# Optimization experiments

Hardware: AMD Instinct MI355X
Metric: run time of the kernel (lower is better)

Reference implementation:

```python
import jax, jax.numpy as jnp
import numpy as np

D_MODEL = 1024
D_FF = 4096
NUM_EXPERTS = 8
TOP_K = 2


def setup_inputs() -> dict:
    key = jax.random.key(0)
    ks = jax.random.split(key, 7)
    s = 1.0 / np.sqrt(D_MODEL)
    sf = 1.0 / np.sqrt(D_FF)
    x = jax.random.normal(ks[0], (4, 2048, D_MODEL), dtype=jnp.float32)
    gate_w = jax.random.uniform(ks[1], (D_MODEL, NUM_EXPERTS), minval=-s, maxval=s, dtype=jnp.float32)
    gate_b = jnp.zeros((NUM_EXPERTS,), dtype=jnp.float32)
    w1 = jax.random.uniform(ks[2], (NUM_EXPERTS, D_MODEL, D_FF), minval=-s, maxval=s, dtype=jnp.float32)
    b1 = jax.random.uniform(ks[3], (NUM_EXPERTS, D_FF), minval=-s, maxval=s, dtype=jnp.float32)
    w2 = jax.random.uniform(ks[4], (NUM_EXPERTS, D_FF, D_MODEL), minval=-sf, maxval=sf, dtype=jnp.float32)
    b2 = jax.random.uniform(ks[5], (NUM_EXPERTS, D_MODEL), minval=-sf, maxval=sf, dtype=jnp.float32)
    return {"x": x, "gate_w": gate_w, "gate_b": gate_b, "w1": w1, "b1": b1, "w2": w2, "b2": b2}


def reference(x, gate_w, gate_b, w1, b1, w2, b2):
    # Router: softmax over experts, then top-k with renormalization.
    router_logits = jnp.einsum('bsd,de->bse', x, gate_w) + gate_b  # [B,S,E]
    router_probs = jax.nn.softmax(router_logits, axis=-1)
    topk_probs, topk_idx = jax.lax.top_k(router_probs, TOP_K)      # [B,S,K]
    topk_probs = topk_probs / jnp.sum(topk_probs, axis=-1, keepdims=True)

    # Dense combine weights: comb[b,s,e] = sum_k topk_probs[b,s,k] * (topk_idx[b,s,k]==e)
    one_hot = jax.nn.one_hot(topk_idx, NUM_EXPERTS, dtype=x.dtype)  # [B,S,K,E]
    comb = jnp.einsum('bsk,bske->bse', topk_probs, one_hot)         # [B,S,E]

    # Loop over the small fixed expert set; weight unselected experts by 0.
    out = jnp.zeros_like(x)
    for e in range(NUM_EXPERTS):
        h = jax.nn.relu(jnp.einsum('bsd,df->bsf', x, w1[e]) + b1[e])
        y = jnp.einsum('bsf,fd->bsd', h, w2[e]) + b2[e]
        out = out + comb[..., e:e + 1] * y

    # Routing statistics (same math as the torch module).
    expert_usage = jnp.mean(one_hot, axis=(0, 1, 2))  # fraction of (token,k) slots per expert
    avg_probs = jnp.mean(router_probs, axis=(0, 1))
    load_balance_loss = jnp.var(avg_probs, ddof=1)    # torch.var is unbiased by default
    return out, expert_usage, load_balance_loss
```

## Files before the change

### kernel.cpp

```cpp
#include <hip/hip_runtime.h>
#include <hip/hip_bf16.h>
#include <stdint.h>

#define D_MODEL 1024
#define D_FF    4096
#define NE      8
#define NTOK    8192
#define OUT_MAIN (NTOK * D_MODEL)

typedef float f32x4 __attribute__((ext_vector_type(4)));
typedef short s16x8 __attribute__((ext_vector_type(8)));

struct __align__(8) bh4 { __hip_bfloat16 x, y, z, w; };

static const size_t OFF_E12   = 4096;
static const size_t OFF_PFR   = 36864;
static const size_t OFF_ATOK  = 102400;
static const size_t OFF_AP    = 167936;
static const size_t OFF_XB    = 262144;
static const size_t OFF_W1T   = OFF_XB  + (size_t)NTOK * D_MODEL * 2;
static const size_t OFF_W2T   = OFF_W1T + (size_t)NE * D_MODEL * D_FF * 2;
static const size_t OFF_H     = OFF_W2T + (size_t)NE * D_MODEL * D_FF * 2;

__device__ inline void gll16(const void* g, void* lds) {
  __builtin_amdgcn_global_load_lds((__attribute__((address_space(1))) void*)g,
                                   (__attribute__((address_space(3))) void*)lds,
                                   16, 0, 0);
}

__global__ __launch_bounds__(256) void cvt_transpose_kernel(
    const float* __restrict__ src, __hip_bfloat16* __restrict__ dst, int K, int N)
{
  __shared__ __hip_bfloat16 tile[64][68];
  const int e = blockIdx.z;
  const float* s = src + (size_t)e * K * N;
  __hip_bfloat16* d = dst + (size_t)e * K * N;
  const int n0 = blockIdx.x * 64, k0 = blockIdx.y * 64;
  const int t = threadIdx.x;
#pragma unroll
  for (int i = 0; i < 4; ++i) {
    int q = i * 256 + t;
    int r = q >> 4, c4 = (q & 15) * 4;
    float4 v = *(const float4*)(s + (size_t)(k0 + r) * N + n0 + c4);
    tile[r][c4 + 0] = __float2bfloat16(v.x);
    tile[r][c4 + 1] = __float2bfloat16(v.y);
    tile[r][c4 + 2] = __float2bfloat16(v.z);
    tile[r][c4 + 3] = __float2bfloat16(v.w);
  }
  __syncthreads();
  const int n = t >> 2, c = (t & 3) * 16;
  __align__(16) __hip_bfloat16 tmp[16];
#pragma unroll
  for (int j = 0; j < 16; ++j) tmp[j] = tile[c + j][n];
  uint4* tv = (uint4*)tmp;
  __hip_bfloat16* dp = d + (size_t)(n0 + n) * K + k0 + c;
  ((uint4*)dp)[0] = tv[0];
  ((uint4*)dp)[1] = tv[1];
}

__global__ __launch_bounds__(256) void router_kernel(
    const float* __restrict__ x, const float* __restrict__ gw, const float* __restrict__ gb,
    __hip_bfloat16* __restrict__ xb, int* __restrict__ e12, float2* __restrict__ pfr,
    float* __restrict__ blkps)
{
  __shared__ float lps[4][8];
  const int l = threadIdx.x & 63;
  const int w = threadIdx.x >> 6;
  const int t = blockIdx.x * 4 + w;
  const float4* xr = (const float4*)(x + (size_t)t * D_MODEL);
  bh4* xbr = (bh4*)(xb + (size_t)t * D_MODEL);
  float a[8] = {0, 0, 0, 0, 0, 0, 0, 0};
#pragma unroll
  for (int c = 0; c < 4; ++c) {
    int idx = c * 64 + l;
    float4 v = xr[idx];
    bh4 hb;
    hb.x = __float2bfloat16(v.x); hb.y = __float2bfloat16(v.y);
    hb.z = __float2bfloat16(v.z); hb.w = __float2bfloat16(v.w);
    xbr[idx] = hb;
    const float* g = gw + (size_t)idx * 32;
#pragma unroll
    for (int j = 0; j < 4; ++j) {
      float xv = (&v.x)[j];
#pragma unroll
      for (int e = 0; e < 8; ++e) a[e] = fmaf(xv, g[j * 8 + e], a[e]);
    }
  }
#pragma unroll
  for (int e = 0; e < 8; ++e) {
    float s = a[e];
#pragma unroll
    for (int off = 32; off > 0; off >>= 1) s += __shfl_xor(s, off, 64);
    a[e] = s + gb[e];
  }
  float m = a[0];
#pragma unroll
  for (int e = 1; e < 8; ++e) m = fmaxf(m, a[e]);
  float p[8], s = 0.f;
#pragma unroll
  for (int e = 0; e < 8; ++e) { p[e] = expf(a[e] - m); s += p[e]; }
  float inv = 1.0f / s;
#pragma unroll
  for (int e = 0; e < 8; ++e) p[e] *= inv;
  int e1 = 0; float p1 = p[0];
#pragma unroll
  for (int e = 1; e < 8; ++e) if (p[e] > p1) { p1 = p[e]; e1 = e; }
  int e2 = (e1 == 0) ? 1 : 0; float p2 = p[e2];
#pragma unroll
  for (int e = 0; e < 8; ++e) if (e != e1 && p[e] > p2) { p2 = p[e]; e2 = e; }

  if (l < 8) lps[w][l] = p[l];
  if (l == 0) {
    float rs = 1.0f / (p1 + p2);
    e12[t] = e1 | (e2 << 8);
    pfr[t] = make_float2(p1 * rs, p2 * rs);
  }
  __syncthreads();
  if (threadIdx.x < 8)
    blkps[(size_t)blockIdx.x * 8 + threadIdx.x] =
        lps[0][threadIdx.x] + lps[1][threadIdx.x] + lps[2][threadIdx.x] + lps[3][threadIdx.x];
}

__global__ __launch_bounds__(256) void count_kernel(
    const int* __restrict__ e12, int* __restrict__ sblkcnt)
{
  __shared__ int wcnt[4][8];
  const int t = threadIdx.x, b = blockIdx.x, w = t >> 6, l = t & 63;
  int ee = e12[b * 256 + t];
  int e1 = ee & 0xff, e2 = ee >> 8;
#pragma unroll
  for (int k = 0; k < 8; ++k) {
    unsigned long long c1 = __ballot(e1 == k);
    unsigned long long c2 = __ballot(e2 == k);
    if (l == 0) wcnt[w][k] = __popcll(c1) + __popcll(c2);
  }
  __syncthreads();
  if (t < 8) sblkcnt[b * 8 + t] = wcnt[0][t] + wcnt[1][t] + wcnt[2][t] + wcnt[3][t];
}

__global__ __launch_bounds__(256) void finalize_kernel(
    int* __restrict__ ctrl, const float* __restrict__ blkps, const int* __restrict__ sblkcnt,
    int* __restrict__ bases, float* __restrict__ out_tail)
{
  __shared__ float part[256];
  __shared__ float ps[8];
  __shared__ int scnt[8];
  const int t = threadIdx.x;
  const int e = t & 7, ch = t >> 3;
  float s = 0.f;
  for (int i = 0; i < 64; ++i) s += blkps[(size_t)(ch * 64 + i) * 8 + e];
  part[t] = s;
  __syncthreads();
  if (t < 8) {
    float a = 0.f;
    for (int c = 0; c < 32; ++c) a += part[c * 8 + t];
    ps[t] = a;
    int cn = 0;
    for (int b = 0; b < 32; ++b) cn += sblkcnt[b * 8 + t];
    scnt[t] = cn;
    ctrl[t] = cn;
    out_tail[t] = (float)cn * (1.0f / 16384.0f);
  }
  __syncthreads();
  if (t < 8) {
    int eo = 0;
    for (int i = 0; i < t; ++i) eo += scnt[i];
    ctrl[16 + t] = eo;
    int run = eo;
    for (int b = 0; b < 32; ++b) { bases[b * 8 + t] = run; run += sblkcnt[b * 8 + t]; }
    if (t == 0) {
      float mean = 0.f;
      for (int i = 0; i < 8; ++i) mean += ps[i];
      mean *= (1.0f / 8192.0f) * 0.125f;
      float v = 0.f;
      for (int i = 0; i < 8; ++i) { float d = ps[i] * (1.0f / 8192.0f) - mean; v += d * d; }
      out_tail[8] = v * (1.0f / 7.0f);
    }
  }
}

__global__ __launch_bounds__(256) void place_kernel(
    const int* __restrict__ e12, const float2* __restrict__ pfr, const int* __restrict__ bases,
    int* __restrict__ atok, float* __restrict__ ap)
{
  __shared__ int wcnt[4][8];
  const int t = threadIdx.x, b = blockIdx.x, w = t >> 6, l = t & 63;
  int tok = b * 256 + t;
  int ee = e12[tok];
  int e1 = ee & 0xff, e2 = ee >> 8;
  float2 p = pfr[tok];
  unsigned long long myA = 0, myA2 = 0, myB = 0;
#pragma unroll
  for (int k = 0; k < 8; ++k) {
    unsigned long long c1 = __ballot(e1 == k);
    unsigned long long c2 = __ballot(e2 == k);
    if (k == e1) myA = c1;
    if (k == e2) { myA2 = c1; myB = c2; }
    if (l == 0) wcnt[w][k] = __popcll(c1) + __popcll(c2);
  }
  __syncthreads();
  int base1 = bases[b * 8 + e1];
  int base2 = bases[b * 8 + e2];
  for (int w2 = 0; w2 < 4; ++w2) {
    if (w2 < w) { base1 += wcnt[w2][e1]; base2 += wcnt[w2][e2]; }
  }
  unsigned long long below = ((unsigned long long)1 << l) - 1;
  int pos1 = base1 + __popcll(myA & below);
  int pos2 = base2 + __popcll(myA2) + __popcll(myB & below);
  atok[pos1] = tok; ap[pos1] = p.x;
  atok[pos2] = tok; ap[pos2] = p.y;
}

template <bool G1>
__global__ __launch_bounds__(256) void moe_gemm_kernel(
    const __hip_bfloat16* __restrict__ A, const __hip_bfloat16* __restrict__ Bw,
    const float* __restrict__ bias, __hip_bfloat16* __restrict__ Hout,
    float* __restrict__ Oout, const int* __restrict__ ctrl,
    const int* __restrict__ atok, const float* __restrict__ ap)
{
  constexpr int KD = G1 ? D_MODEL : D_FF;
  constexpr int ND = G1 ? D_FF : D_MODEL;
  constexpr int KRUN = G1 ? (KD / 64) : (KD / 128);
  const int e = blockIdx.z;
  const int cte = ctrl[e];
  int mt, ks;
  if constexpr (G1) { mt = blockIdx.y; ks = 0; }
  else              { mt = blockIdx.y >> 1; ks = blockIdx.y & 1; }
  if (mt * 128 >= cte) return;
  const int n0 = blockIdx.x * 128;
  const int slot0 = ctrl[16 + e] + mt * 128;
  int cntLoc = cte - mt * 128; if (cntLoc > 128) cntLoc = 128;

  __shared__ ushort As[128 * 64];
  __shared__ ushort Bs[128 * 64];

  const int t = threadIdx.x, l = t & 63, w = t >> 6;
  const int kbase = ks * (KD / 2);

  const ushort* ag[4];
  const ushort* bg[4];
#pragma unroll
  for (int i = 0; i < 4; ++i) {
    int q = i * 256 + t;
    int row = q >> 3, cl = q & 7, cg = cl ^ (row & 7);
    int rr = row < cntLoc ? row : 0;
    size_t arow;
    if constexpr (G1) arow = (size_t)atok[slot0 + rr] * D_MODEL;
    else              arow = (size_t)(slot0 + rr) * D_FF;
    ag[i] = (const ushort*)A + arow + kbase + cg * 8;
    bg[i] = (const ushort*)Bw + (size_t)e * ND * KD + (size_t)(n0 + row) * KD + kbase + cg * 8;
  }

  f32x4 acc[4][4] = {};
  const int wm = w & 1, wn = w >> 1;
  const int ml = l & 15, kg = l >> 4;

  for (int kt = 0; kt < KRUN; ++kt) {
#pragma unroll
    for (int i = 0; i < 4; ++i) {
      gll16(ag[i], &As[(i * 256 + w * 64) * 8]);
      ag[i] += 64;
    }
#pragma unroll
    for (int i = 0; i < 4; ++i) {
      gll16(bg[i], &Bs[(i * 256 + w * 64) * 8]);
      bg[i] += 64;
    }
    __syncthreads();
#pragma unroll
    for (int kss = 0; kss < 2; ++kss) {
      s16x8 af[4], bf[4];
#pragma unroll
      for (int mi = 0; mi < 4; ++mi) {
        int row = wm * 64 + mi * 16 + ml;
        int c = kss * 4 + kg;
        af[mi] = *(const s16x8*)&As[row * 64 + ((c ^ (row & 7)) * 8)];
      }
#pragma unroll
      for (int ni = 0; ni < 4; ++ni) {
        int row = wn * 64 + ni * 16 + ml;
        int c = kss * 4 + kg;
        bf[ni] = *(const s16x8*)&Bs[row * 64 + ((c ^ (row & 7)) * 8)];
      }
#pragma unroll
      for (int mi = 0; mi < 4; ++mi)
#pragma unroll
        for (int ni = 0; ni < 4; ++ni)
          acc[mi][ni] = __builtin_amdgcn_mfma_f32_16x16x32_bf16(af[mi], bf[ni], acc[mi][ni], 0, 0, 0);
    }
    __syncthreads();
  }

  const int lr = kg * 4, lc = ml;
  if constexpr (G1) {
#pragma unroll
    for (int ni = 0; ni < 4; ++ni) {
      int col = n0 + wn * 64 + ni * 16 + lc;
      float bv = bias[(size_t)e * ND + col];
#pragma unroll
      for (int mi = 0; mi < 4; ++mi) {
#pragma unroll
        for (int r = 0; r < 4; ++r) {
          int rl = wm * 64 + mi * 16 + lr + r;
          if (rl < cntLoc) {
            float vv = fmaxf(acc[mi][ni][r] + bv, 0.0f);
            Hout[(size_t)(slot0 + rl) * D_FF + col] = __float2bfloat16(vv);
          }
        }
      }
    }
  } else {
    float bv[4];
#pragma unroll
    for (int ni = 0; ni < 4; ++ni)
      bv[ni] = (ks == 0) ? bias[(size_t)e * ND + n0 + wn * 64 + ni * 16 + lc] : 0.0f;
#pragma unroll
    for (int mi = 0; mi < 4; ++mi) {
#pragma unroll
      for (int r = 0; r < 4; ++r) {
        int rl = wm * 64 + mi * 16 + lr + r;
        if (rl < cntLoc) {
          int slot = slot0 + rl;
          float p = ap[slot];
          float* orow = Oout + (size_t)atok[slot] * D_MODEL + n0;
#pragma unroll
          for (int ni = 0; ni < 4; ++ni) {
            int colL = wn * 64 + ni * 16 + lc;
            unsafeAtomicAdd(orow + colL, p * (acc[mi][ni][r] + bv[ni]));
          }
        }
      }
    }
  }
}

extern "C" void kernel_launch(void* const* d_in, const int* in_sizes, int n_in,
                              void* d_out, int out_size, void* d_ws, size_t ws_size,
                              hipStream_t stream)
{
  const float* x  = (const float*)d_in[0];
  const float* gw = (const float*)d_in[1];
  const float* gb = (const float*)d_in[2];
  const float* w1 = (const float*)d_in[3];
  const float* b1 = (const float*)d_in[4];
  const float* w2 = (const float*)d_in[5];
  const float* b2 = (const float*)d_in[6];
  float* out = (float*)d_out;
  char* ws = (char*)d_ws;

  int*    ctrl    = (int*)ws;
  int*    bases   = (int*)(ws + 1024);
  int*    sblkcnt = (int*)(ws + 3072);
  int*    e12  = (int*)(ws + OFF_E12);
  float2* pfr  = (float2*)(ws + OFF_PFR);
  int*    atok = (int*)(ws + OFF_ATOK);
  float*  ap   = (float*)(ws + OFF_AP);
  __hip_bfloat16* xb   = (__hip_bfloat16*)(ws + OFF_XB);
  __hip_bfloat16* w1t  = (__hip_bfloat16*)(ws + OFF_W1T);
  __hip_bfloat16* w2t  = (__hip_bfloat16*)(ws + OFF_W2T);
  __hip_bfloat16* hbuf = (__hip_bfloat16*)(ws + OFF_H);
  float*  blkps = (float*)(ws + OFF_H);

  hipMemsetAsync(d_out, 0, (size_t)out_size * sizeof(float), stream);

  cvt_transpose_kernel<<<dim3(D_FF / 64, D_MODEL / 64, NE), 256, 0, stream>>>(w1, w1t, D_MODEL, D_FF);
  cvt_transpose_kernel<<<dim3(D_MODEL / 64, D_FF / 64, NE), 256, 0, stream>>>(w2, w2t, D_FF, D_MODEL);
  router_kernel<<<NTOK / 4, 256, 0, stream>>>(x, gw, gb, xb, e12, pfr, blkps);
  count_kernel<<<NTOK / 256, 256, 0, stream>>>(e12, sblkcnt);
  finalize_kernel<<<1, 256, 0, stream>>>(ctrl, blkps, sblkcnt, bases, out + OUT_MAIN);
  place_kernel<<<NTOK / 256, 256, 0, stream>>>(e12, pfr, bases, atok, ap);
  moe_gemm_kernel<true ><<<dim3(D_FF / 128, 64, NE), 256, 0, stream>>>(xb, w1t, b1, hbuf, nullptr, ctrl, atok, ap);
  moe_gemm_kernel<false><<<dim3(D_MODEL / 128, 128, NE), 256, 0, stream>>>(hbuf, w2t, b2, nullptr, out, ctrl, atok, ap);
}
```

Before: 932.1 us.

## Replace atomic scatter in second GEMM with bf16 staging plus gather-combine kernel

The second expert GEMM no longer splits K in two and scatters results into the output with float atomics. It now writes per-slot bf16 results to a workspace buffer that reuses the w1 transpose region. A new combine kernel recomputes each token's slot positions, then gathers the two expert rows and applies probabilities and b2 bias, which removes the output memset and the atomic contention. The grid is also reordered so the M-tile index is the fastest-varying dimension, which may help B-tile reuse in cache. The cost is an extra kernel, an extra bf16 round-trip of the outputs, and lost parallelism from dropping the K split.

```diff
diff --git a/kernel.cpp b/kernel.cpp
--- a/kernel.cpp
+++ b/kernel.cpp
@@ -16,7 +16,6 @@
 static const size_t OFF_E12   = 4096;
 static const size_t OFF_PFR   = 36864;
 static const size_t OFF_ATOK  = 102400;
-static const size_t OFF_AP    = 167936;
 static const size_t OFF_XB    = 262144;
 static const size_t OFF_W1T   = OFF_XB  + (size_t)NTOK * D_MODEL * 2;
 static const size_t OFF_W2T   = OFF_W1T + (size_t)NE * D_MODEL * D_FF * 2;
@@ -26,6 +25,10 @@
   __builtin_amdgcn_global_load_lds((__attribute__((address_space(1))) void*)g,
                                    (__attribute__((address_space(3))) void*)lds,
                                    16, 0, 0);
+}
+
+__device__ inline float bf2f(ushort u) {
+  union { uint i; float f; } v; v.i = (uint)u << 16; return v.f;
 }
 
 __global__ __launch_bounds__(256) void cvt_transpose_kernel(
@@ -180,15 +183,13 @@
 }
 
 __global__ __launch_bounds__(256) void place_kernel(
-    const int* __restrict__ e12, const float2* __restrict__ pfr, const int* __restrict__ bases,
-    int* __restrict__ atok, float* __restrict__ ap)
+    const int* __restrict__ e12, const int* __restrict__ bases, int* __restrict__ atok)
 {
   __shared__ int wcnt[4][8];
   const int t = threadIdx.x, b = blockIdx.x, w = t >> 6, l = t & 63;
   int tok = b * 256 + t;
   int ee = e12[tok];
   int e1 = ee & 0xff, e2 = ee >> 8;
-  float2 p = pfr[tok];
   unsigned long long myA = 0, myA2 = 0, myB = 0;
 #pragma unroll
   for (int k = 0; k < 8; ++k) {
@@ -207,27 +208,24 @@
   unsigned long long below = ((unsigned long long)1 << l) - 1;
   int pos1 = base1 + __popcll(myA & below);
   int pos2 = base2 + __popcll(myA2) + __popcll(myB & below);
-  atok[pos1] = tok; ap[pos1] = p.x;
-  atok[pos2] = tok; ap[pos2] = p.y;
+  atok[pos1] = tok;
+  atok[pos2] = tok;
 }
 
 template <bool G1>
 __global__ __launch_bounds__(256) void moe_gemm_kernel(
     const __hip_bfloat16* __restrict__ A, const __hip_bfloat16* __restrict__ Bw,
     const float* __restrict__ bias, __hip_bfloat16* __restrict__ Hout,
-    float* __restrict__ Oout, const int* __restrict__ ctrl,
-    const int* __restrict__ atok, const float* __restrict__ ap)
+    const int* __restrict__ ctrl, const int* __restrict__ atok)
 {
   constexpr int KD = G1 ? D_MODEL : D_FF;
   constexpr int ND = G1 ? D_FF : D_MODEL;
-  constexpr int KRUN = G1 ? (KD / 64) : (KD / 128);
+  constexpr int KRUN = KD / 64;
   const int e = blockIdx.z;
   const int cte = ctrl[e];
-  int mt, ks;
-  if constexpr (G1) { mt = blockIdx.y; ks = 0; }
-  else              { mt = blockIdx.y >> 1; ks = blockIdx.y & 1; }
+  const int mt = blockIdx.x;
   if (mt * 128 >= cte) return;
-  const int n0 = blockIdx.x * 128;
+  const int n0 = blockIdx.y * 128;
   const int slot0 = ctrl[16 + e] + mt * 128;
   int cntLoc = cte - mt * 128; if (cntLoc > 128) cntLoc = 128;
 
@@ -235,7 +233,6 @@
   __shared__ ushort Bs[128 * 64];
 
   const int t = threadIdx.x, l = t & 63, w = t >> 6;
-  const int kbase = ks * (KD / 2);
 
   const ushort* ag[4];
   const ushort* bg[4];
@@ -247,8 +244,8 @@
     size_t arow;
     if constexpr (G1) arow = (size_t)atok[slot0 + rr] * D_MODEL;
     else              arow = (size_t)(slot0 + rr) * D_FF;
-    ag[i] = (const ushort*)A + arow + kbase + cg * 8;
-    bg[i] = (const ushort*)Bw + (size_t)e * ND * KD + (size_t)(n0 + row) * KD + kbase + cg * 8;
+    ag[i] = (const ushort*)A + arow + cg * 8;
+    bg[i] = (const ushort*)Bw + (size_t)e * ND * KD + (size_t)(n0 + row) * KD + cg * 8;
   }
 
   f32x4 acc[4][4] = {};
@@ -310,27 +307,80 @@
       }
     }
   } else {
-    float bv[4];
-#pragma unroll
-    for (int ni = 0; ni < 4; ++ni)
-      bv[ni] = (ks == 0) ? bias[(size_t)e * ND + n0 + wn * 64 + ni * 16 + lc] : 0.0f;
-#pragma unroll
-    for (int mi = 0; mi < 4; ++mi) {
-#pragma unroll
-      for (int r = 0; r < 4; ++r) {
-        int rl = wm * 64 + mi * 16 + lr + r;
-        if (rl < cntLoc) {
-          int slot = slot0 + rl;
-          float p = ap[slot];
-          float* orow = Oout + (size_t)atok[slot] * D_MODEL + n0;
-#pragma unroll
-          for (int ni = 0; ni < 4; ++ni) {
-            int colL = wn * 64 + ni * 16 + lc;
-            unsafeAtomicAdd(orow + colL, p * (acc[mi][ni][r] + bv[ni]));
-          }
+#pragma unroll
+    for (int ni = 0; ni < 4; ++ni) {
+      int col = n0 + wn * 64 + ni * 16 + lc;
+#pragma unroll
+      for (int mi = 0; mi < 4; ++mi) {
+#pragma unroll
+        for (int r = 0; r < 4; ++r) {
+          int rl = wm * 64 + mi * 16 + lr + r;
+          if (rl < cntLoc)
+            Hout[(size_t)(slot0 + rl) * D_MODEL + col] = __float2bfloat16(acc[mi][ni][r]);
         }
       }
     }
+  }
+}
+
+__global__ __launch_bounds__(256) void combine_kernel(
+    const int* __restrict__ e12, const float2* __restrict__ pfr, const int* __restrict__ bases,
+    const __hip_bfloat16* __restrict__ ybuf, const float* __restrict__ b2,
+    float* __restrict__ out)
+{
+  __shared__ int wcnt[4][8];
+  __shared__ int spos1[256], spos2[256];
+  __shared__ float sp1[256], sp2[256];
+  __shared__ uchar2 se[256];
+  __shared__ float b2l[8][128];
+  const int t = threadIdx.x, b = blockIdx.x, w = t >> 6, l = t & 63;
+  const int c0 = blockIdx.y * 128;
+  int tok = b * 256 + t;
+  int ee = e12[tok];
+  int e1 = ee & 0xff, e2 = ee >> 8;
+  float2 p = pfr[tok];
+  unsigned long long myA = 0, myA2 = 0, myB = 0;
+#pragma unroll
+  for (int k = 0; k < 8; ++k) {
+    unsigned long long c1 = __ballot(e1 == k);
+    unsigned long long c2 = __ballot(e2 == k);
+    if (k == e1) myA = c1;
+    if (k == e2) { myA2 = c1; myB = c2; }
+    if (l == 0) wcnt[w][k] = __popcll(c1) + __popcll(c2);
+  }
+  __syncthreads();
+  int base1 = bases[b * 8 + e1];
+  int base2 = bases[b * 8 + e2];
+  for (int w2 = 0; w2 < 4; ++w2) {
+    if (w2 < w) { base1 += wcnt[w2][e1]; base2 += wcnt[w2][e2]; }
+  }
+  unsigned long long below = ((unsigned long long)1 << l) - 1;
+  spos1[t] = base1 + __popcll(myA & below);
+  spos2[t] = base2 + __popcll(myA2) + __popcll(myB & below);
+  sp1[t] = p.x; sp2[t] = p.y;
+  se[t] = make_uchar2((unsigned char)e1, (unsigned char)e2);
+  {
+    int idx = t * 4;
+    *(float4*)&b2l[idx >> 7][idx & 127] = *(const float4*)&b2[(size_t)(idx >> 7) * D_MODEL + c0 + (idx & 127)];
+  }
+  __syncthreads();
+  const int tsub = t >> 5;
+  const int lc4 = (t & 31) * 4;
+  for (int j = 0; j < 32; ++j) {
+    int jt = j * 8 + tsub;
+    int q1 = spos1[jt], q2 = spos2[jt];
+    float pa = sp1[jt], pb = sp2[jt];
+    uchar2 es = se[jt];
+    ushort4 ya = *(const ushort4*)((const ushort*)ybuf + (size_t)q1 * D_MODEL + c0 + lc4);
+    ushort4 yb = *(const ushort4*)((const ushort*)ybuf + (size_t)q2 * D_MODEL + c0 + lc4);
+    const float* ba = &b2l[es.x][lc4];
+    const float* bb = &b2l[es.y][lc4];
+    float4 o;
+    o.x = pa * (bf2f(ya.x) + ba[0]) + pb * (bf2f(yb.x) + bb[0]);
+    o.y = pa * (bf2f(ya.y) + ba[1]) + pb * (bf2f(yb.y) + bb[1]);
+    o.z = pa * (bf2f(ya.z) + ba[2]) + pb * (bf2f(yb.z) + bb[2]);
+    o.w = pa * (bf2f(ya.w) + ba[3]) + pb * (bf2f(yb.w) + bb[3]);
+    *(float4*)&out[(size_t)(b * 256 + jt) * D_MODEL + c0 + lc4] = o;
   }
 }
 
@@ -354,21 +404,20 @@
   int*    e12  = (int*)(ws + OFF_E12);
   float2* pfr  = (float2*)(ws + OFF_PFR);
   int*    atok = (int*)(ws + OFF_ATOK);
-  float*  ap   = (float*)(ws + OFF_AP);
   __hip_bfloat16* xb   = (__hip_bfloat16*)(ws + OFF_XB);
   __hip_bfloat16* w1t  = (__hip_bfloat16*)(ws + OFF_W1T);
   __hip_bfloat16* w2t  = (__hip_bfloat16*)(ws + OFF_W2T);
   __hip_bfloat16* hbuf = (__hip_bfloat16*)(ws + OFF_H);
   float*  blkps = (float*)(ws + OFF_H);
-
-  hipMemsetAsync(d_out, 0, (size_t)out_size * sizeof(float), stream);
+  __hip_bfloat16* ybuf = (__hip_bfloat16*)(ws + OFF_W1T);
 
   cvt_transpose_kernel<<<dim3(D_FF / 64, D_MODEL / 64, NE), 256, 0, stream>>>(w1, w1t, D_MODEL, D_FF);
   cvt_transpose_kernel<<<dim3(D_MODEL / 64, D_FF / 64, NE), 256, 0, stream>>>(w2, w2t, D_FF, D_MODEL);
   router_kernel<<<NTOK / 4, 256, 0, stream>>>(x, gw, gb, xb, e12, pfr, blkps);
   count_kernel<<<NTOK / 256, 256, 0, stream>>>(e12, sblkcnt);
   finalize_kernel<<<1, 256, 0, stream>>>(ctrl, blkps, sblkcnt, bases, out + OUT_MAIN);
-  place_kernel<<<NTOK / 256, 256, 0, stream>>>(e12, pfr, bases, atok, ap);
-  moe_gemm_kernel<true ><<<dim3(D_FF / 128, 64, NE), 256, 0, stream>>>(xb, w1t, b1, hbuf, nullptr, ctrl, atok, ap);
-  moe_gemm_kernel<false><<<dim3(D_MODEL / 128, 128, NE), 256, 0, stream>>>(hbuf, w2t, b2, nullptr, out, ctrl, atok, ap);
-}
+  place_kernel<<<NTOK / 256, 256, 0, stream>>>(e12, bases, atok);
+  moe_gemm_kernel<true ><<<dim3(64, D_FF / 128, NE), 256, 0, stream>>>(xb, w1t, b1, hbuf, ctrl, atok);
+  moe_gemm_kernel<false><<<dim3(64, D_MODEL / 128, NE), 256, 0, stream>>>(hbuf, w2t, nullptr, ybuf, ctrl, atok);
+  combine_kernel<<<dim3(NTOK / 256, 8), 256, 0, stream>>>(e12, pfr, bases, ybuf, b2, out);
+}
```

Result: slower. 1.187 ms (+27.3%).
